# Kernel optimization log

Measured on AMD Instinct MI355X. Metric: run time of the kernel, lower is better.

The kernel has to match this reference:

```python
import jax, jax.numpy as jnp
import numpy as np

N, E, F_IN, HID, OUT, N_ROOTS = 100000, 1600000, 128, 128, 64, 1024


def _lin_params(key, fan_in, fan_out):
    k1, k2 = jax.random.split(key)
    s = 1.0 / np.sqrt(fan_in)
    w = jax.random.uniform(k1, (fan_in, fan_out), jnp.float32, -s, s)
    b = jax.random.uniform(k2, (fan_out,), jnp.float32, -s, s)
    return w, b


def setup_inputs() -> dict:
    key = jax.random.key(0)
    ks = jax.random.split(key, 16)
    x = jax.random.normal(ks[0], (N, F_IN), jnp.float32)
    edge_index = jax.random.randint(ks[1], (2, E), 0, N, jnp.int64)
    root_idx = jax.random.randint(ks[2], (N_ROOTS,), 0, N, jnp.int64)
    # GINConv MLPs: Linear(in,out) -> ReLU -> Linear(out,out); train_eps=True (init 0)
    w0a, b0a = _lin_params(ks[3], F_IN, HID)
    w0b, b0b = _lin_params(ks[4], HID, HID)
    w1a, b1a = _lin_params(ks[5], HID, HID)
    w1b, b1b = _lin_params(ks[6], HID, HID)
    w2a, b2a = _lin_params(ks[7], HID, OUT)
    w2b, b2b = _lin_params(ks[8], OUT, OUT)
    z = jnp.zeros((), jnp.float32)
    return dict(x=x, edge_index=edge_index, root_idx=root_idx,
                eps0=z, w0a=w0a, b0a=b0a, w0b=w0b, b0b=b0b,
                eps1=z, w1a=w1a, b1a=b1a, w1b=w1b, b1b=b1b,
                eps2=z, w2a=w2a, b2a=b2a, w2b=w2b, b2b=b2b)


def _gin_conv(x, edge_index, eps, w1, b1, w2, b2):
    src, dst = edge_index[0], edge_index[1]
    # sum_{j in N(i)} x_j : gather source features, scatter-add to destinations
    agg = jax.ops.segment_sum(x[src], dst, num_segments=x.shape[0])
    h = (1.0 + eps) * x + agg
    h = jnp.maximum(h @ w1 + b1, 0.0)
    return h @ w2 + b2


def reference(x, edge_index, root_idx,
              eps0, w0a, b0a, w0b, b0b,
              eps1, w1a, b1a, w1b, b1b,
              eps2, w2a, b2a, w2b, b2b):
    h = jnp.maximum(_gin_conv(x, edge_index, eps0, w0a, b0a, w0b, b0b), 0.0)
    h = jnp.maximum(_gin_conv(h, edge_index, eps1, w1a, b1a, w1b, b1b), 0.0)
    # dropout is identity at inference (self.training == False)
    h = _gin_conv(h, edge_index, eps2, w2a, b2a, w2b, b2b)
    return h[root_idx]  # [N_ROOTS, OUT] == x[root_mask]
```

## Files before the change

### kernel.cpp

```cpp
#include <hip/hip_runtime.h>


typedef __bf16  bf16x8 __attribute__((ext_vector_type(8)));
typedef float   f32x4  __attribute__((ext_vector_type(4)));

#define NBINS 784
#define BCAP  38
#define CAP   8192
#define LDR   136

__global__ __launch_bounds__(256) void k_cvt_x(const float4* __restrict__ in,
                                               unsigned short* __restrict__ outb,
                                               long n8) {
    long i = (long)blockIdx.x * 256 + threadIdx.x;
    if (i >= n8) return;
    float4 a = in[2 * i], b = in[2 * i + 1];
    bf16x8 v;
    v[0] = (__bf16)a.x; v[1] = (__bf16)a.y; v[2] = (__bf16)a.z; v[3] = (__bf16)a.w;
    v[4] = (__bf16)b.x; v[5] = (__bf16)b.y; v[6] = (__bf16)b.z; v[7] = (__bf16)b.w;
    *(bf16x8*)&outb[i * 8] = v;
}

__global__ __launch_bounds__(256) void k_cvt_w4(const float* __restrict__ wa,
                                                const float* __restrict__ wb,
                                                const float* __restrict__ wc,
                                                const float* __restrict__ wd,
                                                unsigned short* __restrict__ out) {
    int i = blockIdx.x * 256 + threadIdx.x;
    int m = i >> 14, j = i & 16383;
    const float* w = (m == 0) ? wa : (m == 1) ? wb : (m == 2) ? wc : wd;
    int k = j >> 7, n = j & 127;
    *(__bf16*)&out[m * 16384 + n * 128 + k] = (__bf16)w[j];
}

__global__ __launch_bounds__(1024) void k_scatter(const int* __restrict__ src,
                                                  const int* __restrict__ dst,
                                                  int* __restrict__ gcnt,
                                                  int* __restrict__ realcnt,
                                                  unsigned* __restrict__ ebuf,
                                                  int e, int nb) {
    __shared__ unsigned lbuf[NBINS * BCAP];
    __shared__ int lcnt[NBINS];
    __shared__ int sbase[NBINS];
    const int t = threadIdx.x;
    for (int b = t; b < nb; b += 1024) lcnt[b] = 0;
    __syncthreads();

    const int per = (((e + 255) / 256) + 7) & ~7;
    const int beg = blockIdx.x * per;
    const int end = (beg + per < e) ? beg + per : e;

    for (int base = beg; base < end; base += 8192) {
        int i0 = base + t * 8;
        if (i0 >= end) continue;
        if (i0 + 8 <= end) {
            int4 s0 = *(const int4*)&src[i0];
            int4 s1 = *(const int4*)&src[i0 + 4];
            int4 d0 = *(const int4*)&dst[i0];
            int4 d1 = *(const int4*)&dst[i0 + 4];
            int ss[8] = {s0.x, s0.y, s0.z, s0.w, s1.x, s1.y, s1.z, s1.w};
            int dd[8] = {d0.x, d0.y, d0.z, d0.w, d1.x, d1.y, d1.z, d1.w};
#pragma unroll
            for (int q = 0; q < 8; ++q) {
                int b = dd[q] >> 7;
                int p = atomicAdd(&lcnt[b], 1);
                if (p < BCAP)
                    lbuf[b * BCAP + p] =
                        (unsigned)ss[q] | ((unsigned)(dd[q] & 127) << 17);
            }
        } else {
            int lim = (i0 + 8 < end) ? i0 + 8 : end;
            for (int i = i0; i < lim; ++i) {
                int d = dst[i];
                int b = d >> 7;
                int p = atomicAdd(&lcnt[b], 1);
                if (p < BCAP)
                    lbuf[b * BCAP + p] =
                        (unsigned)src[i] | ((unsigned)(d & 127) << 17);
            }
        }
    }
    __syncthreads();

    for (int b = t; b < nb; b += 1024) {
        int r = lcnt[b]; if (r > BCAP) r = BCAP;
        int bb = 0;
        if (r > 0) {
            int nf = (r + 15) & ~15;
            bb = atomicAdd(&gcnt[b * 16], nf);
            atomicAdd(&realcnt[b], r);
        }
        sbase[b] = bb;
    }
    __syncthreads();

    const int wave = t >> 6, lane = t & 63;
    const int gidx = wave * 4 + (lane >> 4), sub = lane & 15;
    for (int b = gidx; b < nb; b += 64) {
        int r = lcnt[b]; if (r > BCAP) r = BCAP;
        if (r == 0) continue;
        int nf = (r + 15) & ~15;
        int base2 = sbase[b];
        unsigned* cell = ebuf + (size_t)b * CAP;
        for (int j = sub; j < nf; j += 16) {
            unsigned v = (j < r) ? lbuf[b * BCAP + j] : 0xFFFFFFFFu;
            if (base2 + j < CAP) cell[base2 + j] = v;
        }
    }
}

__global__ __launch_bounds__(1024) void k_bscan(const int* __restrict__ realcnt,
                                                int* __restrict__ boff,
                                                int* __restrict__ rp,
                                                int nb, int n, int e) {
    __shared__ int sh[1024];
    int t = threadIdx.x;
    sh[t] = (t < nb) ? realcnt[t] : 0;
    __syncthreads();
    for (int off = 1; off < 1024; off <<= 1) {
        int u = (t >= off) ? sh[t - off] : 0;
        __syncthreads();
        sh[t] += u;
        __syncthreads();
    }
    if (t < nb) boff[t] = (t == 0) ? 0 : sh[t - 1];
    if (t == 0) rp[n] = e;
}

__global__ __launch_bounds__(512) void k_build(const unsigned* __restrict__ ebuf,
                                               const int* __restrict__ gcnt,
                                               const int* __restrict__ boff,
                                               int* __restrict__ rp,
                                               int* __restrict__ csr, int n) {
    __shared__ int bins[128];
    __shared__ int incl[128];
    __shared__ int cur[128];
    int b = blockIdx.x, t = threadIdx.x;
    if (t < 128) bins[t] = 0;
    __syncthreads();
    int c = gcnt[b * 16]; if (c > CAP) c = CAP;
    const unsigned* seg = ebuf + ((size_t)b * CAP);
    for (int j = t; j < c; j += 512) {
        unsigned w = seg[j];
        if (w != 0xFFFFFFFFu) atomicAdd(&bins[(w >> 17) & 127], 1);
    }
    __syncthreads();
    if (t < 128) incl[t] = bins[t];
    __syncthreads();
    for (int off = 1; off < 128; off <<= 1) {
        int u = (t < 128 && t >= off) ? incl[t - off] : 0;
        __syncthreads();
        if (t < 128) incl[t] += u;
        __syncthreads();
    }
    int base = boff[b];
    if (t < 128) {
        int ex = (t == 0) ? 0 : incl[t - 1];
        cur[t] = ex;
        int node = b * 128 + t;
        if (node < n) rp[node] = base + ex;
    }
    __syncthreads();
    for (int j = t; j < c; j += 512) {
        unsigned w = seg[j];
        if (w != 0xFFFFFFFFu) {
            int slot = atomicAdd(&cur[(w >> 17) & 127], 1);
            csr[base + slot] = (int)(w & 0x1FFFF);
        }
    }
}

__global__ void k_flag(const int* __restrict__ roots, int nr,
                       const int* __restrict__ rp, const int* __restrict__ csr,
                       int* __restrict__ af) {
    int i = blockIdx.x * blockDim.x + threadIdx.x;
    if (i >= nr) return;
    int r = roots[i];
    af[r] = 1;
    int e = rp[r + 1];
    for (int k = rp[r]; k < e; ++k) af[csr[k]] = 1;
}

__global__ void k_compact(const int* __restrict__ af, int* __restrict__ list,
                          int* __restrict__ cnt, int n) {
    int i = blockIdx.x * blockDim.x + threadIdx.x;
    if (i < n && af[i]) {
        int p = atomicAdd(cnt, 1);
        list[p] = i;
    }
}

__global__ __launch_bounds__(256) void k_segz(const unsigned short* __restrict__ xb,
                                              const int* __restrict__ rp,
                                              const int* __restrict__ csr,
                                              const float* __restrict__ epsp,
                                              unsigned short* __restrict__ zout,
                                              const int* __restrict__ list,
                                              const int* __restrict__ cntp, int n) {
    int gid = blockIdx.x * 256 + threadIdx.x;
    int j = gid >> 4, lane = gid & 15;
    int rows = n;
    if (cntp) { int c = *cntp; rows = c < n ? c : n; }
    if (j >= rows) return;
    int node = list ? list[j] : j;
    int b = rp[node], e = rp[node + 1];
    float s0[8], s1[8];
#pragma unroll
    for (int q = 0; q < 8; ++q) { s0[q] = 0.f; s1[q] = 0.f; }
    int k = b;
    for (; k + 1 < e; k += 2) {
        bf16x8 v0 = *(const bf16x8*)&xb[(size_t)csr[k]     * 128 + lane * 8];
        bf16x8 v1 = *(const bf16x8*)&xb[(size_t)csr[k + 1] * 128 + lane * 8];
#pragma unroll
        for (int q = 0; q < 8; ++q) { s0[q] += (float)v0[q]; s1[q] += (float)v1[q]; }
    }
    if (k < e) {
        bf16x8 v0 = *(const bf16x8*)&xb[(size_t)csr[k] * 128 + lane * 8];
#pragma unroll
        for (int q = 0; q < 8; ++q) s0[q] += (float)v0[q];
    }
    const float epsv = 1.0f + epsp[0];
    bf16x8 xv = *(const bf16x8*)&xb[(size_t)node * 128 + lane * 8];
    bf16x8 o;
#pragma unroll
    for (int q = 0; q < 8; ++q)
        o[q] = (__bf16)(epsv * (float)xv[q] + s0[q] + s1[q]);
    *(bf16x8*)&zout[(size_t)j * 128 + lane * 8] = o;
}

__global__ __launch_bounds__(256) void k_mlp(const unsigned short* __restrict__ zbuf,
                                             const unsigned short* __restrict__ w1T,
                                             const float* __restrict__ b1,
                                             const unsigned short* __restrict__ w2T,
                                             const float* __restrict__ b2,
                                             unsigned short* __restrict__ out,
                                             const int* __restrict__ list,
                                             const int* __restrict__ cntp, int nrows) {
    __shared__ unsigned short zt[128 * LDR];
    const int t = threadIdx.x;
    int rows = nrows;
    if (cntp) { int c = *cntp; rows = c < nrows ? c : nrows; }
    const int row0 = blockIdx.x * 128;
    if (row0 >= rows) return;

    for (int i = t; i < 2048; i += 256) {
        int r = i >> 4, c = i & 15;
        int g = row0 + r;
        bf16x8 zv;
        if (g < rows) {
            zv = *(const bf16x8*)&zbuf[(size_t)g * 128 + c * 8];
        } else {
#pragma unroll
            for (int q = 0; q < 8; ++q) zv[q] = (__bf16)0.0f;
        }
        *(bf16x8*)&zt[r * LDR + c * 8] = zv;
    }
    __syncthreads();

    const int lane = t & 63;
    const int wm = (t >> 7) & 1, wn = (t >> 6) & 1;
    const int lr = lane & 15, lk = lane >> 4;

    f32x4 zero4 = {0.f, 0.f, 0.f, 0.f};
    f32x4 acc[4][4];
#pragma unroll
    for (int mt = 0; mt < 4; ++mt)
#pragma unroll
        for (int nt = 0; nt < 4; ++nt) acc[mt][nt] = zero4;

#pragma unroll
    for (int kb = 0; kb < 4; ++kb) {
        const int c = kb * 4 + lk;
        bf16x8 a[4];
#pragma unroll
        for (int mt = 0; mt < 4; ++mt)
            a[mt] = *(const bf16x8*)&zt[(wm * 64 + mt * 16 + lr) * LDR + c * 8];
#pragma unroll
        for (int nt = 0; nt < 4; ++nt) {
            bf16x8 b = *(const bf16x8*)&w1T[(wn * 64 + nt * 16 + lr) * 128 + c * 8];
#pragma unroll
            for (int mt = 0; mt < 4; ++mt)
                acc[mt][nt] = __builtin_amdgcn_mfma_f32_16x16x32_bf16(a[mt], b, acc[mt][nt], 0, 0, 0);
        }
    }
    __syncthreads();

#pragma unroll
    for (int nt = 0; nt < 4; ++nt) {
        int col = wn * 64 + nt * 16 + lr;
        float bv = b1[col];
#pragma unroll
        for (int mt = 0; mt < 4; ++mt)
#pragma unroll
            for (int q = 0; q < 4; ++q) {
                int hr = wm * 64 + mt * 16 + lk * 4 + q;
                float hv = fmaxf(acc[mt][nt][q] + bv, 0.f);
                *(__bf16*)&zt[hr * LDR + col] = (__bf16)hv;
            }
    }
    __syncthreads();

    f32x4 acc2[4][4];
#pragma unroll
    for (int mt = 0; mt < 4; ++mt)
#pragma unroll
        for (int nt = 0; nt < 4; ++nt) acc2[mt][nt] = zero4;
#pragma unroll
    for (int kb = 0; kb < 4; ++kb) {
        const int c = kb * 4 + lk;
        bf16x8 a[4];
#pragma unroll
        for (int mt = 0; mt < 4; ++mt)
            a[mt] = *(const bf16x8*)&zt[(wm * 64 + mt * 16 + lr) * LDR + c * 8];
#pragma unroll
        for (int nt = 0; nt < 4; ++nt) {
            bf16x8 b = *(const bf16x8*)&w2T[(wn * 64 + nt * 16 + lr) * 128 + c * 8];
#pragma unroll
            for (int mt = 0; mt < 4; ++mt)
                acc2[mt][nt] = __builtin_amdgcn_mfma_f32_16x16x32_bf16(a[mt], b, acc2[mt][nt], 0, 0, 0);
        }
    }
    __syncthreads();

#pragma unroll
    for (int nt = 0; nt < 4; ++nt) {
        int col = wn * 64 + nt * 16 + lr;
        float bv = b2[col];
#pragma unroll
        for (int mt = 0; mt < 4; ++mt)
#pragma unroll
            for (int q = 0; q < 4; ++q) {
                int orow = wm * 64 + mt * 16 + lk * 4 + q;
                float ov = fmaxf(acc2[mt][nt][q] + bv, 0.f);
                *(__bf16*)&zt[orow * LDR + col] = (__bf16)ov;
            }
    }
    __syncthreads();

    for (int i = t; i < 2048; i += 256) {
        int r = i >> 4, c = i & 15;
        int g = row0 + r;
        if (g < rows) {
            int node = list ? list[g] : g;
            *(bf16x8*)&out[(size_t)node * 128 + c * 8] =
                *(const bf16x8*)&zt[r * LDR + c * 8];
        }
    }
}

__global__ __launch_bounds__(128) void k_root(const unsigned short* __restrict__ x2,
                                              const int* __restrict__ rp,
                                              const int* __restrict__ csr,
                                              const int* __restrict__ roots,
                                              const float* __restrict__ epsp,
                                              const float* __restrict__ wa,
                                              const float* __restrict__ ba,
                                              const float* __restrict__ wb,
                                              const float* __restrict__ bb,
                                              float* __restrict__ out) {
    __shared__ float hin[128];
    __shared__ float h[64];
    int r = blockIdx.x, t = threadIdx.x;
    int node = roots[r];
    float s = (1.0f + epsp[0]) * (float)(*(const __bf16*)&x2[(size_t)node * 128 + t]);
    int b = rp[node], e = rp[node + 1];
    for (int k = b; k < e; ++k)
        s += (float)(*(const __bf16*)&x2[(size_t)csr[k] * 128 + t]);
    hin[t] = s;
    __syncthreads();
    if (t < 64) {
        float a = ba[t];
        for (int k = 0; k < 128; ++k) a += hin[k] * wa[k * 64 + t];
        h[t] = fmaxf(a, 0.f);
    }
    __syncthreads();
    if (t < 64) {
        float a = bb[t];
        for (int k = 0; k < 64; ++k) a += h[k] * wb[k * 64 + t];
        out[(size_t)r * 64 + t] = a;
    }
}

extern "C" void kernel_launch(void* const* d_in, const int* in_sizes, int n_in,
                              void* d_out, int out_size, void* d_ws, size_t ws_size,
                              hipStream_t stream) {
    const float* x    = (const float*)d_in[0];
    const int*   ei   = (const int*)d_in[1];
    const int*   root = (const int*)d_in[2];
    const float* eps0 = (const float*)d_in[3];
    const float* w0a  = (const float*)d_in[4];
    const float* b0a  = (const float*)d_in[5];
    const float* w0b  = (const float*)d_in[6];
    const float* b0b  = (const float*)d_in[7];
    const float* eps1 = (const float*)d_in[8];
    const float* w1a  = (const float*)d_in[9];
    const float* b1a  = (const float*)d_in[10];
    const float* w1b  = (const float*)d_in[11];
    const float* b1b  = (const float*)d_in[12];
    const float* eps2 = (const float*)d_in[13];
    const float* w2a  = (const float*)d_in[14];
    const float* b2a  = (const float*)d_in[15];
    const float* w2b  = (const float*)d_in[16];
    const float* b2b  = (const float*)d_in[17];

    const int N  = in_sizes[0] / 128;
    const int E  = in_sizes[1] / 2;
    const int NR = in_sizes[2];
    const int MAXACT = 65536;
    const int NB = (N + 127) / 128;
    const int* src = ei;
    const int* dst = ei + E;

    char* p = (char*)d_ws;
    unsigned short* xb = (unsigned short*)p; p += (size_t)N * 128 * 2;
    unsigned short* x1 = (unsigned short*)p; p += (size_t)N * 128 * 2;
    unsigned short* z0 = (unsigned short*)p; p += (size_t)N * 128 * 2;
    char* shared0 = p;
    size_t ebuf_bytes = (size_t)NB * CAP * 4;
    size_t x2_bytes   = (size_t)N * 128 * 2;
    p += (ebuf_bytes > x2_bytes ? ebuf_bytes : x2_bytes);
    unsigned*       ebuf = (unsigned*)shared0;
    unsigned short* x2   = (unsigned short*)shared0;
    unsigned short* z1   = (unsigned short*)p; p += (size_t)MAXACT * 128 * 2;
    unsigned short* wT   = (unsigned short*)p; p += 4 * 128 * 128 * 2;
    int* rp      = (int*)p; p += (size_t)(N + 64) * 4;
    int* list    = (int*)p; p += (size_t)(N + 64) * 4;
    int* boff    = (int*)p; p += 4096;
    char* zbeg = p;
    int* af      = (int*)p; p += (size_t)(N + 64) * 4;
    int* cnt     = (int*)p; p += 256;
    int* gcnt    = (int*)p; p += (size_t)NB * 16 * 4;
    int* realcnt = (int*)p; p += (size_t)(NB + 64) * 4;
    size_t zbytes = (size_t)(p - zbeg);
    int* csr     = (int*)p; p += (size_t)E * 4;
    unsigned short* w0aT = wT;
    unsigned short* w0bT = wT + 16384;
    unsigned short* w1aT = wT + 32768;
    unsigned short* w1bT = wT + 49152;

    k_cvt_x<<<(N * 128 / 8 + 255) / 256, 256, 0, stream>>>((const float4*)x, xb, (long)N * 16);
    k_cvt_w4<<<256, 256, 0, stream>>>(w0a, w0b, w1a, w1b, wT);

    hipMemsetAsync(zbeg, 0, zbytes, stream);
    k_scatter<<<256, 1024, 0, stream>>>(src, dst, gcnt, realcnt, ebuf, E, NB);
    k_bscan<<<1, 1024, 0, stream>>>(realcnt, boff, rp, NB, N, E);
    k_build<<<NB, 512, 0, stream>>>(ebuf, gcnt, boff, rp, csr, N);

    k_flag<<<(NR + 255) / 256, 256, 0, stream>>>(root, NR, rp, csr, af);
    k_compact<<<(N + 255) / 256, 256, 0, stream>>>(af, list, cnt, N);

    k_segz<<<(N * 16 + 255) / 256, 256, 0, stream>>>(xb, rp, csr, eps0, z0,
                                                     nullptr, nullptr, N);
    k_mlp<<<(N + 127) / 128, 256, 0, stream>>>(z0, w0aT, b0a, w0bT, b0b,
                                               x1, nullptr, nullptr, N);
    k_segz<<<(MAXACT * 16 + 255) / 256, 256, 0, stream>>>(x1, rp, csr, eps1, z1,
                                                          list, cnt, MAXACT);
    k_mlp<<<(MAXACT + 127) / 128, 256, 0, stream>>>(z1, w1aT, b1a, w1bT, b1b,
                                                    x2, list, cnt, MAXACT);
    k_root<<<NR, 128, 0, stream>>>(x2, rp, csr, root, eps2, w2a, b2a, w2b, b2b,
                                   (float*)d_out);
}
```

Measured before the change: 229.1 us.

## Fold conversions and root flagging into scatter and CSR build kernels

Moves the x and weight bf16 conversions and root marking into the scatter kernel's prologue, removing two separate launches. Neighbor flagging of roots now happens inside the CSR build kernel via a per-bin isroot table, which removes the serial per-root k_flag pass. This cuts launch overhead and the latency of k_flag's serial neighbor loop. In exchange, the scatter kernel's 256 blocks of 1024 threads must do the bulk x conversion before their scatter work starts, which could lengthen that kernel.

```diff
diff --git a/kernel.cpp b/kernel.cpp
--- a/kernel.cpp
+++ b/kernel.cpp
@@ -8,42 +8,50 @@
 #define BCAP  38
 #define CAP   8192
 #define LDR   136
-
-__global__ __launch_bounds__(256) void k_cvt_x(const float4* __restrict__ in,
-                                               unsigned short* __restrict__ outb,
-                                               long n8) {
-    long i = (long)blockIdx.x * 256 + threadIdx.x;
-    if (i >= n8) return;
-    float4 a = in[2 * i], b = in[2 * i + 1];
-    bf16x8 v;
-    v[0] = (__bf16)a.x; v[1] = (__bf16)a.y; v[2] = (__bf16)a.z; v[3] = (__bf16)a.w;
-    v[4] = (__bf16)b.x; v[5] = (__bf16)b.y; v[6] = (__bf16)b.z; v[7] = (__bf16)b.w;
-    *(bf16x8*)&outb[i * 8] = v;
-}
-
-__global__ __launch_bounds__(256) void k_cvt_w4(const float* __restrict__ wa,
-                                                const float* __restrict__ wb,
-                                                const float* __restrict__ wc,
-                                                const float* __restrict__ wd,
-                                                unsigned short* __restrict__ out) {
-    int i = blockIdx.x * 256 + threadIdx.x;
-    int m = i >> 14, j = i & 16383;
-    const float* w = (m == 0) ? wa : (m == 1) ? wb : (m == 2) ? wc : wd;
-    int k = j >> 7, n = j & 127;
-    *(__bf16*)&out[m * 16384 + n * 128 + k] = (__bf16)w[j];
-}
 
 __global__ __launch_bounds__(1024) void k_scatter(const int* __restrict__ src,
                                                   const int* __restrict__ dst,
                                                   int* __restrict__ gcnt,
                                                   int* __restrict__ realcnt,
                                                   unsigned* __restrict__ ebuf,
-                                                  int e, int nb) {
+                                                  int e, int nb,
+                                                  const float4* __restrict__ xf,
+                                                  unsigned short* __restrict__ xb,
+                                                  long n8,
+                                                  const float* __restrict__ w0a,
+                                                  const float* __restrict__ w0b,
+                                                  const float* __restrict__ w1a,
+                                                  const float* __restrict__ w1b,
+                                                  unsigned short* __restrict__ wT,
+                                                  const int* __restrict__ roots,
+                                                  int nr,
+                                                  int* __restrict__ af_root) {
     __shared__ unsigned lbuf[NBINS * BCAP];
     __shared__ int lcnt[NBINS];
     __shared__ int sbase[NBINS];
     const int t = threadIdx.x;
     for (int b = t; b < nb; b += 1024) lcnt[b] = 0;
+
+    {
+        int gi = blockIdx.x * 1024 + t;
+        if (gi < nr) af_root[roots[gi]] = 1;
+    }
+    {
+        int gi = blockIdx.x * 1024 + t;
+        if (gi < 65536) {
+            int m = gi >> 14, j = gi & 16383;
+            const float* w = (m == 0) ? w0a : (m == 1) ? w0b : (m == 2) ? w1a : w1b;
+            int k = j >> 7, n = j & 127;
+            *(__bf16*)&wT[m * 16384 + n * 128 + k] = (__bf16)w[j];
+        }
+    }
+    for (long i = (long)blockIdx.x * 1024 + t; i < n8; i += 262144) {
+        float4 a = xf[2 * i], b = xf[2 * i + 1];
+        bf16x8 v;
+        v[0] = (__bf16)a.x; v[1] = (__bf16)a.y; v[2] = (__bf16)a.z; v[3] = (__bf16)a.w;
+        v[4] = (__bf16)b.x; v[5] = (__bf16)b.y; v[6] = (__bf16)b.z; v[7] = (__bf16)b.w;
+        *(bf16x8*)&xb[i * 8] = v;
+    }
     __syncthreads();
 
     const int per = (((e + 255) / 256) + 7) & ~7;
@@ -131,12 +139,21 @@
                                                const int* __restrict__ gcnt,
                                                const int* __restrict__ boff,
                                                int* __restrict__ rp,
-                                               int* __restrict__ csr, int n) {
+                                               int* __restrict__ csr,
+                                               const int* __restrict__ af_root,
+                                               int* __restrict__ af, int n) {
     __shared__ int bins[128];
     __shared__ int incl[128];
     __shared__ int cur[128];
+    __shared__ unsigned char isroot[128];
     int b = blockIdx.x, t = threadIdx.x;
-    if (t < 128) bins[t] = 0;
+    if (t < 128) {
+        bins[t] = 0;
+        int node = b * 128 + t;
+        unsigned char ir = (node < n && af_root[node]) ? 1 : 0;
+        isroot[t] = ir;
+        if (ir) af[node] = 1;
+    }
     __syncthreads();
     int c = gcnt[b * 16]; if (c > CAP) c = CAP;
     const unsigned* seg = ebuf + ((size_t)b * CAP);
@@ -164,21 +181,13 @@
     for (int j = t; j < c; j += 512) {
         unsigned w = seg[j];
         if (w != 0xFFFFFFFFu) {
-            int slot = atomicAdd(&cur[(w >> 17) & 127], 1);
-            csr[base + slot] = (int)(w & 0x1FFFF);
-        }
-    }
-}
-
-__global__ void k_flag(const int* __restrict__ roots, int nr,
-                       const int* __restrict__ rp, const int* __restrict__ csr,
-                       int* __restrict__ af) {
-    int i = blockIdx.x * blockDim.x + threadIdx.x;
-    if (i >= nr) return;
-    int r = roots[i];
-    af[r] = 1;
-    int e = rp[r + 1];
-    for (int k = rp[r]; k < e; ++k) af[csr[k]] = 1;
+            int ldst = (w >> 17) & 127;
+            int s = (int)(w & 0x1FFFF);
+            int slot = atomicAdd(&cur[ldst], 1);
+            csr[base + slot] = s;
+            if (isroot[ldst]) af[s] = 1;
+        }
+    }
 }
 
 __global__ void k_compact(const int* __restrict__ af, int* __restrict__ list,
@@ -428,6 +437,7 @@
     int* boff    = (int*)p; p += 4096;
     char* zbeg = p;
     int* af      = (int*)p; p += (size_t)(N + 64) * 4;
+    int* af_root = (int*)p; p += (size_t)(N + 64) * 4;
     int* cnt     = (int*)p; p += 256;
     int* gcnt    = (int*)p; p += (size_t)NB * 16 * 4;
     int* realcnt = (int*)p; p += (size_t)(NB + 64) * 4;
@@ -438,15 +448,13 @@
     unsigned short* w1aT = wT + 32768;
     unsigned short* w1bT = wT + 49152;
 
-    k_cvt_x<<<(N * 128 / 8 + 255) / 256, 256, 0, stream>>>((const float4*)x, xb, (long)N * 16);
-    k_cvt_w4<<<256, 256, 0, stream>>>(w0a, w0b, w1a, w1b, wT);
-
     hipMemsetAsync(zbeg, 0, zbytes, stream);
-    k_scatter<<<256, 1024, 0, stream>>>(src, dst, gcnt, realcnt, ebuf, E, NB);
+    k_scatter<<<256, 1024, 0, stream>>>(src, dst, gcnt, realcnt, ebuf, E, NB,
+                                        (const float4*)x, xb, (long)N * 16,
+                                        w0a, w0b, w1a, w1b, wT,
+                                        root, NR, af_root);
     k_bscan<<<1, 1024, 0, stream>>>(realcnt, boff, rp, NB, N, E);
-    k_build<<<NB, 512, 0, stream>>>(ebuf, gcnt, boff, rp, csr, N);
-
-    k_flag<<<(NR + 255) / 256, 256, 0, stream>>>(root, NR, rp, csr, af);
+    k_build<<<NB, 512, 0, stream>>>(ebuf, gcnt, boff, rp, csr, af_root, af, N);
     k_compact<<<(N + 255) / 256, 256, 0, stream>>>(af, list, cnt, N);
 
     k_segz<<<(N * 16 + 255) / 256, 256, 0, stream>>>(xb, rp, csr, eps0, z0,
```

Measured after the change: 212.9 us. 7.1% less time.
